# Optimization experiments

Hardware: AMD Instinct MI355X
Metric: run time of the kernel (lower is better)

## Reference

```python
import jax, jax.numpy as jnp
import numpy as np

N = 100000
E = 1600000
D_IN = 128
D_HID = 128
D_OUT = 64
NUM_LAYERS = 4


def setup_inputs() -> dict:
    key = jax.random.key(0)
    ks = jax.random.split(key, 12)
    features = jax.random.normal(ks[0], (N, D_IN), dtype=jnp.float32)
    edge_index = jax.random.randint(ks[1], (2, E), 0, N, dtype=jnp.int64)
    def glorot(k, shape):
        fan_in, fan_out = shape
        s = jnp.sqrt(6.0 / (fan_in + fan_out)).astype(jnp.float32)
        return jax.random.uniform(k, shape, jnp.float32, -s, s)
    W0 = glorot(ks[2], (D_IN, D_HID)); b0 = jnp.zeros((D_HID,), jnp.float32)
    W1 = glorot(ks[3], (D_HID, D_HID)); b1 = jnp.zeros((D_HID,), jnp.float32)
    W2 = glorot(ks[4], (D_HID, D_HID)); b2 = jnp.zeros((D_HID,), jnp.float32)
    W3 = glorot(ks[5], (D_HID, D_OUT)); b3 = jnp.zeros((D_OUT,), jnp.float32)
    return {"features": features, "edge_index": edge_index,
            "W0": W0, "b0": b0, "W1": W1, "b1": b1,
            "W2": W2, "b2": b2, "W3": W3, "b3": b3}


def _degree_norms(edge_index):
    src, dst = edge_index[0], edge_index[1]
    ones = jnp.ones((src.shape[0],), jnp.float32)
    out_deg = jax.ops.segment_sum(ones, src, num_segments=N)
    in_deg = jax.ops.segment_sum(ones, dst, num_segments=N)
    norm_src = jnp.where(out_deg > 0, jax.lax.rsqrt(jnp.maximum(out_deg, 1.0)), 0.0)
    norm_dst = jnp.where(in_deg > 0, jax.lax.rsqrt(jnp.maximum(in_deg, 1.0)), 0.0)
    return norm_src, norm_dst


def _graph_conv(x, W, b, src, dst, norm_src, norm_dst, act):
    # linear transform first (aggregation is linear, order-equivalent)
    h = x @ W                                   # [N, d_out]
    h = h * norm_src[:, None]                   # symmetric norm, src side
    msg = jnp.take(h, src, axis=0)              # gather  [E, d_out]
    agg = jax.ops.segment_sum(msg, dst, num_segments=N)  # scatter-add [N, d_out]
    agg = agg * norm_dst[:, None]               # symmetric norm, dst side
    agg = agg + b
    if act:
        agg = jnp.tanh(agg)
    return agg


def reference(features, edge_index, W0, b0, W1, b1, W2, b2, W3, b3):
    src, dst = edge_index[0], edge_index[1]
    norm_src, norm_dst = _degree_norms(edge_index)
    x = _graph_conv(features, W0, b0, src, dst, norm_src, norm_dst, act=True)
    x = _graph_conv(x, W1, b1, src, dst, norm_src, norm_dst, act=True)
    x = _graph_conv(x, W2, b2, src, dst, norm_src, norm_dst, act=True)
    x = _graph_conv(x, W3, b3, src, dst, norm_src, norm_dst, act=False)  # last layer: no activation
    return x
```

## Files before the change

kernel.cpp:

```cpp
#include <hip/hip_runtime.h>
#include <cmath>

typedef __attribute__((ext_vector_type(8))) short bf16x8;
typedef __attribute__((ext_vector_type(8))) _Float16 f16x8;
typedef __attribute__((ext_vector_type(4))) float f32x4;

__device__ inline unsigned short f2bf_rne(float f) {
    unsigned int u = __float_as_uint(f);
    unsigned int r = (u + 0x7FFFu + ((u >> 16) & 1u)) >> 16;
    return (unsigned short)r;
}
__device__ inline float bf2f(unsigned short h) {
    return __uint_as_float(((unsigned int)h) << 16);
}

__device__ inline float fast_tanh(float x) {
    float e = x * 2.8853900817779268f;
    e = fminf(fmaxf(e, -126.f), 126.f);
    float t = __builtin_amdgcn_exp2f(e);
    return (t - 1.0f) * __builtin_amdgcn_rcpf(t + 1.0f);
}


constexpr int CB = 256;
constexpr int PREPB = 224;

__global__ __launch_bounds__(256) void k_prep_hist(
        const int* __restrict__ src, const int* __restrict__ dst,
        int* __restrict__ gH, int E, int K, int scanN, int chunk,
        const float* __restrict__ W0, const float* __restrict__ W1,
        const float* __restrict__ W2, const float* __restrict__ W3,
        unsigned short* __restrict__ h0, unsigned short* __restrict__ l0,
        unsigned short* __restrict__ h1, unsigned short* __restrict__ l1,
        unsigned short* __restrict__ h2, unsigned short* __restrict__ l2,
        unsigned short* __restrict__ h3, unsigned short* __restrict__ l3) {
    if (blockIdx.x < CB) {
        extern __shared__ int lds[];
        int* hd = lds; int* hs = lds + K;
        int cb = ((blockIdx.x & 7) * (CB >> 3)) + (blockIdx.x >> 3);
        for (int i = threadIdx.x; i < 2 * K; i += 256) lds[i] = 0;
        __syncthreads();
        int lo = cb * chunk;
        int hi = lo + chunk; if (hi > E) hi = E;
        for (int i = lo + threadIdx.x; i < hi; i += 256) {
            atomicAdd(&hd[dst[i] >> 6], 1);
            atomicAdd(&hs[src[i] >> 6], 1);
        }
        __syncthreads();
        for (int k = threadIdx.x; k < K; k += 256) {
            gH[(size_t)k * CB + cb] = hd[k];
            gH[(size_t)(scanN + k * CB) + cb] = hs[k];
        }
    } else {
        int i = (blockIdx.x - CB) * 256 + threadIdx.x;
        const float* W; unsigned short* wh; unsigned short* wl; int N; int base; bool bf;
        if      (i < 16384) { W = W0; wh = h0; wl = l0; N = 128; base = i;         bf = true;  }
        else if (i < 32768) { W = W1; wh = h1; wl = l1; N = 128; base = i - 16384; bf = false; }
        else if (i < 49152) { W = W2; wh = h2; wl = l2; N = 128; base = i - 32768; bf = false; }
        else if (i < 57344) { W = W3; wh = h3; wl = l3; N = 64;  base = i - 49152; bf = false; }
        else return;
        int n = base >> 7, k = base & 127;
        float w = W[k * N + n];
        if (bf) {
            unsigned short hb = f2bf_rne(w);
            unsigned short lb = f2bf_rne(w - bf2f(hb));
            wh[base] = hb; wl[base] = lb;
        } else {
            union { _Float16 f; unsigned short u; } H, L;
            H.f = (_Float16)w;
            L.f = (_Float16)(w - (float)H.f);
            wh[base] = H.u; wl[base] = L.u;
        }
    }
}

__global__ __launch_bounds__(256) void k_bucket_scatter(const int* __restrict__ src,
                                                        const int* __restrict__ dst,
                                                        const int* __restrict__ gHS,
                                                        int* __restrict__ sortedAll,
                                                        int E, int K, int scanN, int chunk) {
    extern __shared__ int lds[];
    int* bd = lds; int* bs = lds + K;
    int cb = ((blockIdx.x & 7) * (CB >> 3)) + (blockIdx.x >> 3);
    for (int k = threadIdx.x; k < K; k += 256) {
        bd[k] = gHS[(size_t)k * CB + cb];
        bs[k] = gHS[(size_t)(scanN + k * CB) + cb];
    }
    __syncthreads();
    int lo = cb * chunk;
    int hi = lo + chunk; if (hi > E) hi = E;
    for (int i = lo + threadIdx.x; i < hi; i += 256) {
        int d = dst[i], s = src[i];
        int pd = atomicAdd(&bd[d >> 6], 1);
        sortedAll[pd] = ((d & 63) << 17) | s;
        int ps = atomicAdd(&bs[s >> 6], 1);
        sortedAll[ps] = s;
    }
}

constexpr int FINE_CAP = 3072;

__global__ __launch_bounds__(256) void k_fine(const int* __restrict__ sortedAll,
                                              const int* __restrict__ gHS,
                                              int* __restrict__ rowptr,
                                              int* __restrict__ colidx,
                                              float* __restrict__ nsrc,
                                              float* __restrict__ ndst,
                                              int E, int K, int scanN, int N) {
    __shared__ int cnt[64], excl[64], rank[64];
    __shared__ int stage[FINE_CAP];
    int kb = blockIdx.x;
    bool isDst = kb < K;
    int k = isDst ? kb : kb - K;
    int bstart, bend;
    if (isDst) {
        bstart = gHS[(size_t)k * CB];
        bend = (k + 1 < K) ? gHS[(size_t)(k + 1) * CB] : E;
    } else {
        bstart = gHS[(size_t)(scanN + k * CB)];
        bend = (k + 1 < K) ? gHS[(size_t)(scanN + (k + 1) * CB)] : 2 * E;
    }
    int len = bend - bstart;
    bool useLds = isDst && (len <= FINE_CAP);
    if (threadIdx.x < 64) { cnt[threadIdx.x] = 0; rank[threadIdx.x] = 0; }
    if (useLds) {
        for (int i = threadIdx.x; i < len; i += 256)
            stage[i] = sortedAll[bstart + i];
    }
    __syncthreads();
    if (isDst) {
        if (useLds) {
            for (int i = threadIdx.x; i < len; i += 256)
                atomicAdd(&cnt[stage[i] >> 17], 1);
        } else {
            for (int i = bstart + threadIdx.x; i < bend; i += 256)
                atomicAdd(&cnt[sortedAll[i] >> 17], 1);
        }
    } else {
        for (int i = bstart + threadIdx.x; i < bend; i += 256)
            atomicAdd(&cnt[sortedAll[i] & 63], 1);
    }
    __syncthreads();
    if (isDst) {
        if (threadIdx.x == 0) {
            int r = 0;
            for (int j = 0; j < 64; j++) { excl[j] = r; r += cnt[j]; }
        }
        __syncthreads();
        int node0 = k << 6;
        if (threadIdx.x < 64) {
            int node = node0 + threadIdx.x;
            if (node < N) {
                rowptr[node] = bstart + excl[threadIdx.x];
                int c = cnt[threadIdx.x];
                ndst[node] = c > 0 ? rsqrtf((float)c) : 0.f;
            }
        }
        if (k == 0 && threadIdx.x == 0) rowptr[N] = E;
        if (useLds) {
            for (int i = threadIdx.x; i < len; i += 256) {
                int v = stage[i];
                int n = v >> 17;
                int r = atomicAdd(&rank[n], 1);
                colidx[bstart + excl[n] + r] = v & 0x1FFFF;
            }
        } else {
            for (int i = bstart + threadIdx.x; i < bend; i += 256) {
                int v = sortedAll[i];
                int n = v >> 17;
                int r = atomicAdd(&rank[n], 1);
                colidx[bstart + excl[n] + r] = v & 0x1FFFF;
            }
        }
    } else {
        int node = (k << 6) + threadIdx.x;
        if (threadIdx.x < 64 && node < N) {
            int c = cnt[threadIdx.x];
            nsrc[node] = c > 0 ? rsqrtf((float)c) : 0.f;
        }
    }
}


constexpr int SCAN_TILE = 2048;

__global__ __launch_bounds__(256) void k_scan_partial(const int* __restrict__ deg,
                                                      int* __restrict__ tilesum, int n) {
    __shared__ int red[256];
    int base = blockIdx.x * SCAN_TILE;
    int s = 0;
    for (int i = threadIdx.x; i < SCAN_TILE; i += 256) {
        int idx = base + i;
        if (idx < n) s += deg[idx];
    }
    red[threadIdx.x] = s;
    __syncthreads();
    for (int off = 128; off > 0; off >>= 1) {
        if (threadIdx.x < off) red[threadIdx.x] += red[threadIdx.x + off];
        __syncthreads();
    }
    if (threadIdx.x == 0) tilesum[blockIdx.x] = red[0];
}

__global__ __launch_bounds__(256) void k_scan_final(const int* __restrict__ deg,
                                                    const int* __restrict__ tilesum,
                                                    int* __restrict__ outArr, int n) {
    __shared__ int red[256];
    __shared__ int sbase;
    int s0 = 0;
    for (int i = threadIdx.x; i < (int)blockIdx.x; i += 256) s0 += tilesum[i];
    red[threadIdx.x] = s0;
    __syncthreads();
    for (int off = 128; off > 0; off >>= 1) {
        if (threadIdx.x < off) red[threadIdx.x] += red[threadIdx.x + off];
        __syncthreads();
    }
    if (threadIdx.x == 0) sbase = red[0];
    __syncthreads();

    int base = blockIdx.x * SCAN_TILE;
    int lo = base + threadIdx.x * 8;
    int v[8]; int s = 0;
#pragma unroll
    for (int j = 0; j < 8; j++) {
        int idx = lo + j;
        v[j] = (idx < n) ? deg[idx] : 0;
        s += v[j];
    }
    red[threadIdx.x] = s;
    __syncthreads();
    for (int off = 1; off < 256; off <<= 1) {
        int x = red[threadIdx.x];
        int add = (threadIdx.x >= off) ? red[threadIdx.x - off] : 0;
        __syncthreads();
        red[threadIdx.x] = x + add;
        __syncthreads();
    }
    int excl = sbase + (threadIdx.x ? red[threadIdx.x - 1] : 0);
#pragma unroll
    for (int j = 0; j < 8; j++) {
        int idx = lo + j;
        if (idx < n) outArr[idx] = excl;
        excl += v[j];
    }
}


template <int DOUT, int SRC>
__global__ __launch_bounds__(256) void k_gemm_hyb(
        const float* __restrict__ xf, const _Float16* __restrict__ xq,
        const unsigned short* __restrict__ wth, const unsigned short* __restrict__ wtl,
        const float* __restrict__ nsrc, _Float16* __restrict__ h, int nrows) {
    constexpr int NT = DOUT / 16;
    constexpr int LDK = 72;
    __shared__ unsigned short Bh[DOUT * LDK], Bl[DOUT * LDK];

    int tid = threadIdx.x;
    int lane = tid & 63;
    int wv = tid >> 6;
    int quad = lane >> 4, l16 = lane & 15;
    int r0 = blockIdx.x * 64 + wv * 16;
    int rowA = r0 + l16; if (rowA >= nrows) rowA = nrows - 1;

    if (blockIdx.x == 0 && tid < DOUT / 8) {
        f32x4 z = {0.f, 0.f, 0.f, 0.f};
        *(f32x4*)((char*)h + ((size_t)nrows * DOUT + tid * 8) * 2) = z;
    }

    f32x4 acc[NT];
#pragma unroll
    for (int nt = 0; nt < NT; nt++) acc[nt] = (f32x4){0.f, 0.f, 0.f, 0.f};

    for (int kh = 0; kh < 2; kh++) {
        if (kh) __syncthreads();
        for (int i = tid; i < DOUT * 16; i += 256) {
            int n = i >> 4, kb = i & 15;
            int koff = kh * 64 + kb * 4;
            *(ushort4*)&Bh[n * LDK + kb * 4] = *(const ushort4*)&wth[n * 128 + koff];
            *(ushort4*)&Bl[n * LDK + kb * 4] = *(const ushort4*)&wtl[n * 128 + koff];
        }
        __syncthreads();

#pragma unroll
        for (int kq = 0; kq < 2; kq++) {
            int koA = kh * 64 + kq * 32 + quad * 8;
            int koB = kq * 32 + quad * 8;
            if (SRC == 0) {
                const float* xp = &xf[(size_t)rowA * 128 + koA];
                f32x4 x0 = *(const f32x4*)xp;
                f32x4 x1 = *(const f32x4*)(xp + 4);
                union { bf16x8 v; unsigned short u[8]; } H, L;
                float xs[8] = {x0[0], x0[1], x0[2], x0[3], x1[0], x1[1], x1[2], x1[3]};
#pragma unroll
                for (int j = 0; j < 8; j++) {
                    H.u[j] = f2bf_rne(xs[j]);
                    L.u[j] = f2bf_rne(xs[j] - bf2f(H.u[j]));
                }
                bf16x8 ah = H.v, al = L.v;
#pragma unroll
                for (int nt = 0; nt < NT; nt++) {
                    int n = nt * 16 + l16;
                    bf16x8 bh = *(const bf16x8*)&Bh[n * LDK + koB];
                    bf16x8 bl = *(const bf16x8*)&Bl[n * LDK + koB];
                    acc[nt] = __builtin_amdgcn_mfma_f32_16x16x32_bf16(ah, bh, acc[nt], 0, 0, 0);
                    acc[nt] = __builtin_amdgcn_mfma_f32_16x16x32_bf16(ah, bl, acc[nt], 0, 0, 0);
                    acc[nt] = __builtin_amdgcn_mfma_f32_16x16x32_bf16(al, bh, acc[nt], 0, 0, 0);
                }
            } else {
                f16x8 aq = *(const f16x8*)&xq[(size_t)rowA * 128 + koA];
#pragma unroll
                for (int nt = 0; nt < NT; nt++) {
                    int n = nt * 16 + l16;
                    f16x8 bh = *(const f16x8*)&Bh[n * LDK + koB];
                    f16x8 bl = *(const f16x8*)&Bl[n * LDK + koB];
                    acc[nt] = __builtin_amdgcn_mfma_f32_16x16x32_f16(aq, bh, acc[nt], 0, 0, 0);
                    acc[nt] = __builtin_amdgcn_mfma_f32_16x16x32_f16(aq, bl, acc[nt], 0, 0, 0);
                }
            }
        }
    }

#pragma unroll
    for (int r = 0; r < 4; r++) {
        int row = r0 + quad * 4 + r;
        if (row < nrows) {
            float nm = nsrc[row];
#pragma unroll
            for (int nt = 0; nt < NT; nt++)
                h[(size_t)row * DOUT + nt * 16 + l16] = (_Float16)(acc[nt][r] * nm);
        }
    }
}


template <int D, int MODE>
__global__ __launch_bounds__(256) void k_aggregate(const _Float16* __restrict__ h,
                                                   const int* __restrict__ rowptr,
                                                   const int* __restrict__ colidx,
                                                   const float* __restrict__ ndst,
                                                   const float* __restrict__ bias,
                                                   float* __restrict__ out,
                                                   _Float16* __restrict__ oq,
                                                   int n) {
    constexpr int FB = D / 8;
    constexpr int GN = 64 / FB;
    constexpr int EU = 4;
    int wid  = (blockIdx.x * 256 + threadIdx.x) >> 6;
    int lane = threadIdx.x & 63;
    int fb = lane & (FB - 1);
    int g  = lane / FB;
    int waveCount = gridDim.x * 4;

    for (int nbase = wid * GN; nbase < n; nbase += waveCount * GN) {
        int node = nbase + g;
        bool vn = node < n;
        int beg = vn ? rowptr[node] : 0;
        int end = vn ? rowptr[node + 1] : 0;
        int m = end - beg;

        int mmax = m;
#pragma unroll
        for (int off = FB; off < 64; off <<= 1) {
            int t = __shfl_xor(mmax, off);
            mmax = mmax > t ? mmax : t;
        }

        float acc[8];
#pragma unroll
        for (int k = 0; k < 8; k++) acc[k] = 0.f;

        int cv = 0;
        for (int j0 = 0; j0 < mmax; j0 += EU) {
            if ((j0 & (FB - 1)) == 0) {
                int idx = beg + j0 + fb;
                cv = __builtin_nontemporal_load(&colidx[idx < end ? idx : 0]);
            }
            int s[EU];
#pragma unroll
            for (int u = 0; u < EU; u++) {
                int j = j0 + u;
                int sv = __shfl(cv, g * FB + (j & (FB - 1)));
                s[u] = j < m ? sv : n;
            }
            f16x8 v[EU];
#pragma unroll
            for (int u = 0; u < EU; u++)
                v[u] = *(const f16x8*)&h[(size_t)s[u] * D + fb * 8];
#pragma unroll
            for (int u = 0; u < EU; u++) {
#pragma unroll
                for (int k = 0; k < 8; k++)
                    acc[k] += (float)v[u][k];
            }
        }

        if (vn) {
            float nd = ndst[node];
            float bv[8];
            *(float4*)&bv[0] = ((const float4*)bias)[fb * 2];
            *(float4*)&bv[4] = ((const float4*)bias)[fb * 2 + 1];
            float vv[8];
#pragma unroll
            for (int k = 0; k < 8; k++) vv[k] = acc[k] * nd + bv[k];
            if (MODE == 1) {
                f16x8 q;
#pragma unroll
                for (int k = 0; k < 8; k++)
                    q[k] = (_Float16)fast_tanh(vv[k]);
                *(f16x8*)&oq[(size_t)node * D + fb * 8] = q;
            } else {
                *(float4*)&out[(size_t)node * D + fb * 8] = *(float4*)&vv[0];
                *(float4*)&out[(size_t)node * D + fb * 8 + 4] = *(float4*)&vv[4];
            }
        }
    }
}


extern "C" void kernel_launch(void* const* d_in, const int* in_sizes, int n_in,
                              void* d_out, int out_size, void* d_ws, size_t ws_size,
                              hipStream_t stream) {
    const float* features = (const float*)d_in[0];
    const int* edges      = (const int*)d_in[1];
    const float* W0 = (const float*)d_in[2]; const float* b0 = (const float*)d_in[3];
    const float* W1 = (const float*)d_in[4]; const float* b1 = (const float*)d_in[5];
    const float* W2 = (const float*)d_in[6]; const float* b2 = (const float*)d_in[7];
    const float* W3 = (const float*)d_in[8]; const float* b3 = (const float*)d_in[9];
    float* out = (float*)d_out;

    const int N = in_sizes[0] / 128;
    const int E = in_sizes[1] / 2;
    const int* src = edges;
    const int* dst = edges + E;
    const int K = (N + 63) >> 6;
    const int chunk = (E + CB - 1) / CB;
    const int scanN = K * CB;
    const int n2 = 2 * scanN;
    const int numTiles = (n2 + SCAN_TILE - 1) / SCAN_TILE;
    const size_t dynLds = (size_t)2 * K * sizeof(int);

    char* p = (char*)d_ws;
    _Float16* bufH         = (_Float16*)p;       p += (size_t)N * 128 * 4;
    _Float16* xq           = (_Float16*)p;       p += (size_t)(N + 1) * 128 * 2;
    char*     xspare       = p;                  p += (size_t)(N + 1) * 128 * 2;
    int*   rowptr = (int*)p;   p += (((size_t)(N + 1) * 4 + 15) / 16) * 16;
    int*   colidx = (int*)p;   p += (size_t)E * 4;
    float* nsrc   = (float*)p; p += (size_t)N * 4;
    float* ndst   = (float*)p; p += (size_t)N * 4;
    int*   tilesum= (int*)p;   p += (((size_t)(numTiles + 1) * 4 + 15) / 16) * 16;
    unsigned short* wt0h = (unsigned short*)p; p += 16384 * 2;
    unsigned short* wt0l = (unsigned short*)p; p += 16384 * 2;
    unsigned short* wt1h = (unsigned short*)p; p += 16384 * 2;
    unsigned short* wt1l = (unsigned short*)p; p += 16384 * 2;
    unsigned short* wt2h = (unsigned short*)p; p += 16384 * 2;
    unsigned short* wt2l = (unsigned short*)p; p += 16384 * 2;
    unsigned short* wt3h = (unsigned short*)p; p += 8192 * 2;
    unsigned short* wt3l = (unsigned short*)p; p += 8192 * 2;

    char* q = (char*)xq;
    int* sortedAll = (int*)q; q += (size_t)2 * E * 4;
    int* gH        = (int*)q; q += (size_t)n2 * 4;
    int* gHS       = (int*)q; q += (size_t)(n2 + 1) * 4;
    (void)xspare;

    k_prep_hist<<<CB + PREPB, 256, dynLds, stream>>>(src, dst, gH, E, K, scanN, chunk,
                                                     W0, W1, W2, W3,
                                                     wt0h, wt0l, wt1h, wt1l,
                                                     wt2h, wt2l, wt3h, wt3l);
    k_scan_partial<<<numTiles, 256, 0, stream>>>(gH, tilesum, n2);
    k_scan_final<<<numTiles, 256, 0, stream>>>(gH, tilesum, gHS, n2);
    k_bucket_scatter<<<CB, 256, dynLds, stream>>>(src, dst, gHS, sortedAll, E, K, scanN, chunk);
    k_fine<<<2 * K, 256, 0, stream>>>(sortedAll, gHS, rowptr, colidx, nsrc, ndst, E, K, scanN, N);

    int gblk = (N + 63) / 64;
    int ablk128 = (N + 15) / 16;
    int ablk64  = (N + 31) / 32;
    k_gemm_hyb<128, 0><<<gblk, 256, 0, stream>>>(features, nullptr, wt0h, wt0l, nsrc, bufH, N);
    k_aggregate<128, 1><<<ablk128, 256, 0, stream>>>(bufH, rowptr, colidx, ndst, b0, nullptr, xq, N);
    k_gemm_hyb<128, 1><<<gblk, 256, 0, stream>>>(nullptr, xq, wt1h, wt1l, nsrc, bufH, N);
    k_aggregate<128, 1><<<ablk128, 256, 0, stream>>>(bufH, rowptr, colidx, ndst, b1, nullptr, xq, N);
    k_gemm_hyb<128, 1><<<gblk, 256, 0, stream>>>(nullptr, xq, wt2h, wt2l, nsrc, bufH, N);
    k_aggregate<128, 1><<<ablk128, 256, 0, stream>>>(bufH, rowptr, colidx, ndst, b2, nullptr, xq, N);
    k_gemm_hyb<64, 1><<<gblk, 256, 0, stream>>>(nullptr, xq, wt3h, wt3l, nsrc, bufH, N);
    k_aggregate<64, 0><<<ablk64, 256, 0, stream>>>(bufH, rowptr, colidx, ndst, b3, out, nullptr, N);
}
```

Measured before the change: 450.0 us.

## Fuse all GNN layers into one persistent cooperative kernel with grid syncs

```diff
diff --git a/kernel.cpp b/kernel.cpp
--- a/kernel.cpp
+++ b/kernel.cpp
@@ -1,5 +1,8 @@
 #include <hip/hip_runtime.h>
+#include <hip/hip_cooperative_groups.h>
 #include <cmath>
+
+namespace cg = cooperative_groups;
 
 typedef __attribute__((ext_vector_type(8))) short bf16x8;
 typedef __attribute__((ext_vector_type(8))) _Float16 f16x8;
@@ -247,101 +250,104 @@
 
 
 template <int DOUT, int SRC>
-__global__ __launch_bounds__(256) void k_gemm_hyb(
-        const float* __restrict__ xf, const _Float16* __restrict__ xq,
-        const unsigned short* __restrict__ wth, const unsigned short* __restrict__ wtl,
-        const float* __restrict__ nsrc, _Float16* __restrict__ h, int nrows) {
+__device__ void gemm_dev(const float* __restrict__ xf, const _Float16* __restrict__ xq,
+                         const unsigned short* __restrict__ wth,
+                         const unsigned short* __restrict__ wtl,
+                         const float* __restrict__ nsrc, _Float16* __restrict__ h,
+                         int nrows, unsigned short* Bh, unsigned short* Bl, bool zrow) {
     constexpr int NT = DOUT / 16;
     constexpr int LDK = 72;
-    __shared__ unsigned short Bh[DOUT * LDK], Bl[DOUT * LDK];
-
     int tid = threadIdx.x;
     int lane = tid & 63;
     int wv = tid >> 6;
     int quad = lane >> 4, l16 = lane & 15;
-    int r0 = blockIdx.x * 64 + wv * 16;
-    int rowA = r0 + l16; if (rowA >= nrows) rowA = nrows - 1;
-
-    if (blockIdx.x == 0 && tid < DOUT / 8) {
+
+    if (zrow && blockIdx.x == 0 && tid < DOUT / 8) {
         f32x4 z = {0.f, 0.f, 0.f, 0.f};
         *(f32x4*)((char*)h + ((size_t)nrows * DOUT + tid * 8) * 2) = z;
     }
 
-    f32x4 acc[NT];
-#pragma unroll
-    for (int nt = 0; nt < NT; nt++) acc[nt] = (f32x4){0.f, 0.f, 0.f, 0.f};
-
-    for (int kh = 0; kh < 2; kh++) {
-        if (kh) __syncthreads();
-        for (int i = tid; i < DOUT * 16; i += 256) {
-            int n = i >> 4, kb = i & 15;
-            int koff = kh * 64 + kb * 4;
-            *(ushort4*)&Bh[n * LDK + kb * 4] = *(const ushort4*)&wth[n * 128 + koff];
-            *(ushort4*)&Bl[n * LDK + kb * 4] = *(const ushort4*)&wtl[n * 128 + koff];
-        }
-        __syncthreads();
-
-#pragma unroll
-        for (int kq = 0; kq < 2; kq++) {
-            int koA = kh * 64 + kq * 32 + quad * 8;
-            int koB = kq * 32 + quad * 8;
-            if (SRC == 0) {
-                const float* xp = &xf[(size_t)rowA * 128 + koA];
-                f32x4 x0 = *(const f32x4*)xp;
-                f32x4 x1 = *(const f32x4*)(xp + 4);
-                union { bf16x8 v; unsigned short u[8]; } H, L;
-                float xs[8] = {x0[0], x0[1], x0[2], x0[3], x1[0], x1[1], x1[2], x1[3]};
-#pragma unroll
-                for (int j = 0; j < 8; j++) {
-                    H.u[j] = f2bf_rne(xs[j]);
-                    L.u[j] = f2bf_rne(xs[j] - bf2f(H.u[j]));
+    int ntiles = (nrows + 63) >> 6;
+    for (int tile = blockIdx.x; tile < ntiles; tile += gridDim.x) {
+        int r0 = tile * 64 + wv * 16;
+        int rowA = r0 + l16; if (rowA >= nrows) rowA = nrows - 1;
+
+        f32x4 acc[NT];
+#pragma unroll
+        for (int nt = 0; nt < NT; nt++) acc[nt] = (f32x4){0.f, 0.f, 0.f, 0.f};
+
+        for (int kh = 0; kh < 2; kh++) {
+            __syncthreads();
+            for (int i = tid; i < DOUT * 16; i += 256) {
+                int n = i >> 4, kb = i & 15;
+                int koff = kh * 64 + kb * 4;
+                *(ushort4*)&Bh[n * LDK + kb * 4] = *(const ushort4*)&wth[n * 128 + koff];
+                *(ushort4*)&Bl[n * LDK + kb * 4] = *(const ushort4*)&wtl[n * 128 + koff];
+            }
+            __syncthreads();
+
+#pragma unroll
+            for (int kq = 0; kq < 2; kq++) {
+                int koA = kh * 64 + kq * 32 + quad * 8;
+                int koB = kq * 32 + quad * 8;
+                if (SRC == 0) {
+                    const float* xp = &xf[(size_t)rowA * 128 + koA];
+                    f32x4 x0 = *(const f32x4*)xp;
+                    f32x4 x1 = *(const f32x4*)(xp + 4);
+                    union { bf16x8 v; unsigned short u[8]; } H, L;
+                    float xs[8] = {x0[0], x0[1], x0[2], x0[3], x1[0], x1[1], x1[2], x1[3]};
+#pragma unroll
+                    for (int j = 0; j < 8; j++) {
+                        H.u[j] = f2bf_rne(xs[j]);
+                        L.u[j] = f2bf_rne(xs[j] - bf2f(H.u[j]));
+                    }
+                    bf16x8 ah = H.v, al = L.v;
+#pragma unroll
+                    for (int nt = 0; nt < NT; nt++) {
+                        int n = nt * 16 + l16;
+                        bf16x8 bh = *(const bf16x8*)&Bh[n * LDK + koB];
+                        bf16x8 bl = *(const bf16x8*)&Bl[n * LDK + koB];
+                        acc[nt] = __builtin_amdgcn_mfma_f32_16x16x32_bf16(ah, bh, acc[nt], 0, 0, 0);
+                        acc[nt] = __builtin_amdgcn_mfma_f32_16x16x32_bf16(ah, bl, acc[nt], 0, 0, 0);
+                        acc[nt] = __builtin_amdgcn_mfma_f32_16x16x32_bf16(al, bh, acc[nt], 0, 0, 0);
+                    }
+                } else {
+                    f16x8 aq = *(const f16x8*)&xq[(size_t)rowA * 128 + koA];
+#pragma unroll
+                    for (int nt = 0; nt < NT; nt++) {
+                        int n = nt * 16 + l16;
+                        f16x8 bh = *(const f16x8*)&Bh[n * LDK + koB];
+                        f16x8 bl = *(const f16x8*)&Bl[n * LDK + koB];
+                        acc[nt] = __builtin_amdgcn_mfma_f32_16x16x32_f16(aq, bh, acc[nt], 0, 0, 0);
+                        acc[nt] = __builtin_amdgcn_mfma_f32_16x16x32_f16(aq, bl, acc[nt], 0, 0, 0);
+                    }
                 }
-                bf16x8 ah = H.v, al = L.v;
-#pragma unroll
-                for (int nt = 0; nt < NT; nt++) {
-                    int n = nt * 16 + l16;
-                    bf16x8 bh = *(const bf16x8*)&Bh[n * LDK + koB];
-                    bf16x8 bl = *(const bf16x8*)&Bl[n * LDK + koB];
-                    acc[nt] = __builtin_amdgcn_mfma_f32_16x16x32_bf16(ah, bh, acc[nt], 0, 0, 0);
-                    acc[nt] = __builtin_amdgcn_mfma_f32_16x16x32_bf16(ah, bl, acc[nt], 0, 0, 0);
-                    acc[nt] = __builtin_amdgcn_mfma_f32_16x16x32_bf16(al, bh, acc[nt], 0, 0, 0);
-                }
-            } else {
-                f16x8 aq = *(const f16x8*)&xq[(size_t)rowA * 128 + koA];
-#pragma unroll
-                for (int nt = 0; nt < NT; nt++) {
-                    int n = nt * 16 + l16;
-                    f16x8 bh = *(const f16x8*)&Bh[n * LDK + koB];
-                    f16x8 bl = *(const f16x8*)&Bl[n * LDK + koB];
-                    acc[nt] = __builtin_amdgcn_mfma_f32_16x16x32_f16(aq, bh, acc[nt], 0, 0, 0);
-                    acc[nt] = __builtin_amdgcn_mfma_f32_16x16x32_f16(aq, bl, acc[nt], 0, 0, 0);
-                }
-            }
-        }
-    }
-
-#pragma unroll
-    for (int r = 0; r < 4; r++) {
-        int row = r0 + quad * 4 + r;
-        if (row < nrows) {
-            float nm = nsrc[row];
-#pragma unroll
-            for (int nt = 0; nt < NT; nt++)
-                h[(size_t)row * DOUT + nt * 16 + l16] = (_Float16)(acc[nt][r] * nm);
-        }
-    }
-}
-
+            }
+        }
+
+#pragma unroll
+        for (int r = 0; r < 4; r++) {
+            int row = r0 + quad * 4 + r;
+            if (row < nrows) {
+                float nm = nsrc[row];
+#pragma unroll
+                for (int nt = 0; nt < NT; nt++)
+                    h[(size_t)row * DOUT + nt * 16 + l16] = (_Float16)(acc[nt][r] * nm);
+            }
+        }
+        __syncthreads();
+    }
+}
 
 template <int D, int MODE>
-__global__ __launch_bounds__(256) void k_aggregate(const _Float16* __restrict__ h,
-                                                   const int* __restrict__ rowptr,
-                                                   const int* __restrict__ colidx,
-                                                   const float* __restrict__ ndst,
-                                                   const float* __restrict__ bias,
-                                                   float* __restrict__ out,
-                                                   _Float16* __restrict__ oq,
-                                                   int n) {
+__device__ void agg_dev(const _Float16* __restrict__ h,
+                        const int* __restrict__ rowptr,
+                        const int* __restrict__ colidx,
+                        const float* __restrict__ ndst,
+                        const float* __restrict__ bias,
+                        float* __restrict__ out,
+                        _Float16* __restrict__ oq,
+                        int n) {
     constexpr int FB = D / 8;
     constexpr int GN = 64 / FB;
     constexpr int EU = 4;
@@ -414,6 +420,38 @@
             }
         }
     }
+}
+
+__global__ __launch_bounds__(256, 4) void k_net(
+        const float* __restrict__ features, _Float16* __restrict__ xq,
+        _Float16* __restrict__ bufH,
+        const int* __restrict__ rowptr, const int* __restrict__ colidx,
+        const float* __restrict__ nsrc, const float* __restrict__ ndst,
+        const unsigned short* __restrict__ wt0h, const unsigned short* __restrict__ wt0l,
+        const unsigned short* __restrict__ wt1h, const unsigned short* __restrict__ wt1l,
+        const unsigned short* __restrict__ wt2h, const unsigned short* __restrict__ wt2l,
+        const unsigned short* __restrict__ wt3h, const unsigned short* __restrict__ wt3l,
+        const float* __restrict__ b0, const float* __restrict__ b1,
+        const float* __restrict__ b2, const float* __restrict__ b3,
+        float* __restrict__ out, int N) {
+    __shared__ unsigned short Bh[128 * 72], Bl[128 * 72];
+    cg::grid_group grid = cg::this_grid();
+
+    gemm_dev<128, 0>(features, nullptr, wt0h, wt0l, nsrc, bufH, N, Bh, Bl, true);
+    grid.sync();
+    agg_dev<128, 1>(bufH, rowptr, colidx, ndst, b0, nullptr, xq, N);
+    grid.sync();
+    gemm_dev<128, 1>(nullptr, xq, wt1h, wt1l, nsrc, bufH, N, Bh, Bl, false);
+    grid.sync();
+    agg_dev<128, 1>(bufH, rowptr, colidx, ndst, b1, nullptr, xq, N);
+    grid.sync();
+    gemm_dev<128, 1>(nullptr, xq, wt2h, wt2l, nsrc, bufH, N, Bh, Bl, false);
+    grid.sync();
+    agg_dev<128, 1>(bufH, rowptr, colidx, ndst, b2, nullptr, xq, N);
+    grid.sync();
+    gemm_dev<64, 1>(nullptr, xq, wt3h, wt3l, nsrc, bufH, N, Bh, Bl, true);
+    grid.sync();
+    agg_dev<64, 0>(bufH, rowptr, colidx, ndst, b3, out, nullptr, N);
 }
 
 
@@ -472,15 +510,19 @@
     k_bucket_scatter<<<CB, 256, dynLds, stream>>>(src, dst, gHS, sortedAll, E, K, scanN, chunk);
     k_fine<<<2 * K, 256, 0, stream>>>(sortedAll, gHS, rowptr, colidx, nsrc, ndst, E, K, scanN, N);
 
-    int gblk = (N + 63) / 64;
-    int ablk128 = (N + 15) / 16;
-    int ablk64  = (N + 31) / 32;
-    k_gemm_hyb<128, 0><<<gblk, 256, 0, stream>>>(features, nullptr, wt0h, wt0l, nsrc, bufH, N);
-    k_aggregate<128, 1><<<ablk128, 256, 0, stream>>>(bufH, rowptr, colidx, ndst, b0, nullptr, xq, N);
-    k_gemm_hyb<128, 1><<<gblk, 256, 0, stream>>>(nullptr, xq, wt1h, wt1l, nsrc, bufH, N);
-    k_aggregate<128, 1><<<ablk128, 256, 0, stream>>>(bufH, rowptr, colidx, ndst, b1, nullptr, xq, N);
-    k_gemm_hyb<128, 1><<<gblk, 256, 0, stream>>>(nullptr, xq, wt2h, wt2l, nsrc, bufH, N);
-    k_aggregate<128, 1><<<ablk128, 256, 0, stream>>>(bufH, rowptr, colidx, ndst, b2, nullptr, xq, N);
-    k_gemm_hyb<64, 1><<<gblk, 256, 0, stream>>>(nullptr, xq, wt3h, wt3l, nsrc, bufH, N);
-    k_aggregate<64, 0><<<ablk64, 256, 0, stream>>>(bufH, rowptr, colidx, ndst, b3, out, nullptr, N);
-}
+    static int bpc = -1;
+    if (bpc < 0) {
+        hipOccupancyMaxActiveBlocksPerMultiprocessor(&bpc, k_net, 256, 0);
+        if (bpc < 1) bpc = 1;
+    }
+    int grid = bpc * 256;
+    if (grid > 2048) grid = 2048;
+
+    void* args[] = {(void*)&features, (void*)&xq, (void*)&bufH,
+                    (void*)&rowptr, (void*)&colidx, (void*)&nsrc, (void*)&ndst,
+                    (void*)&wt0h, (void*)&wt0l, (void*)&wt1h, (void*)&wt1l,
+                    (void*)&wt2h, (void*)&wt2l, (void*)&wt3h, (void*)&wt3l,
+                    (void*)&b0, (void*)&b1, (void*)&b2, (void*)&b3,
+                    (void*)&out, (void*)&N};
+    hipLaunchCooperativeKernel((const void*)k_net, dim3(grid), dim3(256), args, 0, stream);
+}
```

New measurement: 1.071 ms. 138% more time.

## Split 128-wide hidden features into two 64-column halves for aggregation

Applied to the files above, without the earlier changes.

```diff
diff --git a/kernel.cpp b/kernel.cpp
--- a/kernel.cpp
+++ b/kernel.cpp
@@ -250,7 +250,8 @@
 __global__ __launch_bounds__(256) void k_gemm_hyb(
         const float* __restrict__ xf, const _Float16* __restrict__ xq,
         const unsigned short* __restrict__ wth, const unsigned short* __restrict__ wtl,
-        const float* __restrict__ nsrc, _Float16* __restrict__ h, int nrows) {
+        const float* __restrict__ nsrc, _Float16* __restrict__ h0arr,
+        _Float16* __restrict__ h1arr, int nrows) {
     constexpr int NT = DOUT / 16;
     constexpr int LDK = 72;
     __shared__ unsigned short Bh[DOUT * LDK], Bl[DOUT * LDK];
@@ -264,7 +265,8 @@
 
     if (blockIdx.x == 0 && tid < DOUT / 8) {
         f32x4 z = {0.f, 0.f, 0.f, 0.f};
-        *(f32x4*)((char*)h + ((size_t)nrows * DOUT + tid * 8) * 2) = z;
+        _Float16* hb = (tid < 8) ? h0arr : h1arr;
+        *(f32x4*)((char*)hb + ((size_t)nrows * 64 + (tid & 7) * 8) * 2) = z;
     }
 
     f32x4 acc[NT];
@@ -326,30 +328,36 @@
         if (row < nrows) {
             float nm = nsrc[row];
 #pragma unroll
-            for (int nt = 0; nt < NT; nt++)
-                h[(size_t)row * DOUT + nt * 16 + l16] = (_Float16)(acc[nt][r] * nm);
-        }
-    }
-}
-
-
-template <int D, int MODE>
-__global__ __launch_bounds__(256) void k_aggregate(const _Float16* __restrict__ h,
-                                                   const int* __restrict__ rowptr,
-                                                   const int* __restrict__ colidx,
-                                                   const float* __restrict__ ndst,
-                                                   const float* __restrict__ bias,
-                                                   float* __restrict__ out,
-                                                   _Float16* __restrict__ oq,
-                                                   int n) {
-    constexpr int FB = D / 8;
-    constexpr int GN = 64 / FB;
+            for (int nt = 0; nt < NT; nt++) {
+                _Float16* hb = (DOUT == 128 && nt >= 4) ? h1arr : h0arr;
+                int col = (DOUT == 128 ? (nt & 3) : nt) * 16 + l16;
+                hb[(size_t)row * 64 + col] = (_Float16)(acc[nt][r] * nm);
+            }
+        }
+    }
+}
+
+
+__global__ __launch_bounds__(256) void k_agg128s(const _Float16* __restrict__ h0arr,
+                                                 const _Float16* __restrict__ h1arr,
+                                                 const int* __restrict__ rowptr,
+                                                 const int* __restrict__ colidx,
+                                                 const float* __restrict__ ndst,
+                                                 const float* __restrict__ bias,
+                                                 _Float16* __restrict__ oq,
+                                                 int n) {
+    constexpr int FB = 8;
+    constexpr int GN = 8;
     constexpr int EU = 4;
-    int wid  = (blockIdx.x * 256 + threadIdx.x) >> 6;
+    int half = blockIdx.x & 1;
+    const _Float16* h = half ? h1arr : h0arr;
+    int bidh = blockIdx.x >> 1;
+    int wid  = (bidh * 256 + threadIdx.x) >> 6;
     int lane = threadIdx.x & 63;
     int fb = lane & (FB - 1);
     int g  = lane / FB;
-    int waveCount = gridDim.x * 4;
+    int lbase = lane & ~(FB - 1);
+    int waveCount = (gridDim.x >> 1) * 4;
 
     for (int nbase = wid * GN; nbase < n; nbase += waveCount * GN) {
         int node = nbase + g;
@@ -379,13 +387,87 @@
 #pragma unroll
             for (int u = 0; u < EU; u++) {
                 int j = j0 + u;
-                int sv = __shfl(cv, g * FB + (j & (FB - 1)));
+                int sv = __shfl(cv, lbase + (j & (FB - 1)));
                 s[u] = j < m ? sv : n;
             }
             f16x8 v[EU];
 #pragma unroll
             for (int u = 0; u < EU; u++)
-                v[u] = *(const f16x8*)&h[(size_t)s[u] * D + fb * 8];
+                v[u] = *(const f16x8*)&h[(size_t)s[u] * 64 + fb * 8];
+#pragma unroll
+            for (int u = 0; u < EU; u++) {
+#pragma unroll
+                for (int k = 0; k < 8; k++)
+                    acc[k] += (float)v[u][k];
+            }
+        }
+
+        if (vn) {
+            float nd = ndst[node];
+            float bv[8];
+            *(float4*)&bv[0] = ((const float4*)bias)[half * 16 + fb * 2];
+            *(float4*)&bv[4] = ((const float4*)bias)[half * 16 + fb * 2 + 1];
+            f16x8 q;
+#pragma unroll
+            for (int k = 0; k < 8; k++)
+                q[k] = (_Float16)fast_tanh(acc[k] * nd + bv[k]);
+            *(f16x8*)&oq[(size_t)node * 128 + half * 64 + fb * 8] = q;
+        }
+    }
+}
+
+__global__ __launch_bounds__(256) void k_agg64(const _Float16* __restrict__ h,
+                                               const int* __restrict__ rowptr,
+                                               const int* __restrict__ colidx,
+                                               const float* __restrict__ ndst,
+                                               const float* __restrict__ bias,
+                                               float* __restrict__ out,
+                                               int n) {
+    constexpr int FB = 8;
+    constexpr int GN = 8;
+    constexpr int EU = 4;
+    int wid  = (blockIdx.x * 256 + threadIdx.x) >> 6;
+    int lane = threadIdx.x & 63;
+    int fb = lane & (FB - 1);
+    int g  = lane / FB;
+    int lbase = lane & ~(FB - 1);
+    int waveCount = gridDim.x * 4;
+
+    for (int nbase = wid * GN; nbase < n; nbase += waveCount * GN) {
+        int node = nbase + g;
+        bool vn = node < n;
+        int beg = vn ? rowptr[node] : 0;
+        int end = vn ? rowptr[node + 1] : 0;
+        int m = end - beg;
+
+        int mmax = m;
+#pragma unroll
+        for (int off = FB; off < 64; off <<= 1) {
+            int t = __shfl_xor(mmax, off);
+            mmax = mmax > t ? mmax : t;
+        }
+
+        float acc[8];
+#pragma unroll
+        for (int k = 0; k < 8; k++) acc[k] = 0.f;
+
+        int cv = 0;
+        for (int j0 = 0; j0 < mmax; j0 += EU) {
+            if ((j0 & (FB - 1)) == 0) {
+                int idx = beg + j0 + fb;
+                cv = __builtin_nontemporal_load(&colidx[idx < end ? idx : 0]);
+            }
+            int s[EU];
+#pragma unroll
+            for (int u = 0; u < EU; u++) {
+                int j = j0 + u;
+                int sv = __shfl(cv, lbase + (j & (FB - 1)));
+                s[u] = j < m ? sv : n;
+            }
+            f16x8 v[EU];
+#pragma unroll
+            for (int u = 0; u < EU; u++)
+                v[u] = *(const f16x8*)&h[(size_t)s[u] * 64 + fb * 8];
 #pragma unroll
             for (int u = 0; u < EU; u++) {
 #pragma unroll
@@ -402,16 +484,8 @@
             float vv[8];
 #pragma unroll
             for (int k = 0; k < 8; k++) vv[k] = acc[k] * nd + bv[k];
-            if (MODE == 1) {
-                f16x8 q;
-#pragma unroll
-                for (int k = 0; k < 8; k++)
-                    q[k] = (_Float16)fast_tanh(vv[k]);
-                *(f16x8*)&oq[(size_t)node * D + fb * 8] = q;
-            } else {
-                *(float4*)&out[(size_t)node * D + fb * 8] = *(float4*)&vv[0];
-                *(float4*)&out[(size_t)node * D + fb * 8 + 4] = *(float4*)&vv[4];
-            }
+            *(float4*)&out[(size_t)node * 64 + fb * 8] = *(float4*)&vv[0];
+            *(float4*)&out[(size_t)node * 64 + fb * 8 + 4] = *(float4*)&vv[4];
         }
     }
 }
@@ -440,7 +514,8 @@
     const size_t dynLds = (size_t)2 * K * sizeof(int);
 
     char* p = (char*)d_ws;
-    _Float16* bufH         = (_Float16*)p;       p += (size_t)N * 128 * 4;
+    _Float16* h0buf        = (_Float16*)p;       p += (size_t)(N + 1) * 64 * 2;
+    _Float16* h1buf        = (_Float16*)p;       p += (size_t)(N + 1) * 64 * 2;
     _Float16* xq           = (_Float16*)p;       p += (size_t)(N + 1) * 128 * 2;
     char*     xspare       = p;                  p += (size_t)(N + 1) * 128 * 2;
     int*   rowptr = (int*)p;   p += (((size_t)(N + 1) * 4 + 15) / 16) * 16;
@@ -473,14 +548,14 @@
     k_fine<<<2 * K, 256, 0, stream>>>(sortedAll, gHS, rowptr, colidx, nsrc, ndst, E, K, scanN, N);
 
     int gblk = (N + 63) / 64;
-    int ablk128 = (N + 15) / 16;
+    int ablk128 = 2 * (((N + 7) / 8 + 3) / 4);
     int ablk64  = (N + 31) / 32;
-    k_gemm_hyb<128, 0><<<gblk, 256, 0, stream>>>(features, nullptr, wt0h, wt0l, nsrc, bufH, N);
-    k_aggregate<128, 1><<<ablk128, 256, 0, stream>>>(bufH, rowptr, colidx, ndst, b0, nullptr, xq, N);
-    k_gemm_hyb<128, 1><<<gblk, 256, 0, stream>>>(nullptr, xq, wt1h, wt1l, nsrc, bufH, N);
-    k_aggregate<128, 1><<<ablk128, 256, 0, stream>>>(bufH, rowptr, colidx, ndst, b1, nullptr, xq, N);
-    k_gemm_hyb<128, 1><<<gblk, 256, 0, stream>>>(nullptr, xq, wt2h, wt2l, nsrc, bufH, N);
-    k_aggregate<128, 1><<<ablk128, 256, 0, stream>>>(bufH, rowptr, colidx, ndst, b2, nullptr, xq, N);
-    k_gemm_hyb<64, 1><<<gblk, 256, 0, stream>>>(nullptr, xq, wt3h, wt3l, nsrc, bufH, N);
-    k_aggregate<64, 0><<<ablk64, 256, 0, stream>>>(bufH, rowptr, colidx, ndst, b3, out, nullptr, N);
-}
+    k_gemm_hyb<128, 0><<<gblk, 256, 0, stream>>>(features, nullptr, wt0h, wt0l, nsrc, h0buf, h1buf, N);
+    k_agg128s<<<ablk128, 256, 0, stream>>>(h0buf, h1buf, rowptr, colidx, ndst, b0, xq, N);
+    k_gemm_hyb<128, 1><<<gblk, 256, 0, stream>>>(nullptr, xq, wt1h, wt1l, nsrc, h0buf, h1buf, N);
+    k_agg128s<<<ablk128, 256, 0, stream>>>(h0buf, h1buf, rowptr, colidx, ndst, b1, xq, N);
+    k_gemm_hyb<128, 1><<<gblk, 256, 0, stream>>>(nullptr, xq, wt2h, wt2l, nsrc, h0buf, h1buf, N);
+    k_agg128s<<<ablk128, 256, 0, stream>>>(h0buf, h1buf, rowptr, colidx, ndst, b2, xq, N);
+    k_gemm_hyb<64, 1><<<gblk, 256, 0, stream>>>(nullptr, xq, wt3h, wt3l, nsrc, h0buf, h1buf, N);
+    k_agg64<<<ablk64, 256, 0, stream>>>(h0buf, rowptr, colidx, ndst, b3, out, N);
+}
```

After: 440.3 us. 2.2% less time.
